# Optimization experiments

Hardware: AMD Instinct MI355X
Metric: run time of the kernel (lower is better)

Reference implementation:

```python
import jax, jax.numpy as jnp
from jax import lax
import numpy as np

D_MODEL = 96; D_STATE = 16; SSM_RATIO = 2.0; D_CONV = 3; K = 4
D_INNER = int(SSM_RATIO * D_MODEL)      # 192
DT_RANK = -(-D_MODEL // 16)             # ceil(96/16) = 6
B_SZ = 4; H = 32; W = 32

# ---- zig-zag (snake) index helpers (static numpy) ----
def _snake_h(Hh, Ww):
    idx = np.tile(np.arange(Ww), (Hh, 1)); idx[1::2] = idx[1::2, ::-1]; return idx  # (H,W)

def _snake_v(Hh, Ww):
    idx = np.tile(np.arange(Hh)[:, None], (1, Ww)); idx[:, 1::2] = idx[::-1, 1::2]; return idx  # (H,W)

def _h_scan(x, d):
    Hh, Ww = x.shape[-2:]
    if d == 'left':
        x = jnp.flip(x, (-1, -2))
    return x[:, :, np.arange(Hh)[:, None], _snake_h(Hh, Ww)]

def _v_scan(x, d):
    Bb, Cc, Hh, Ww = x.shape
    if d == 'up':
        x = jnp.flip(x, (-1, -2))
    t = x[:, :, _snake_v(Hh, Ww), np.arange(Ww)[None, :]]  # gather along H per column
    return jnp.swapaxes(t, -1, -2).reshape(Bb, Cc, Hh, Ww)

def _h_merge(x, d):
    Hh, Ww = x.shape[-2:]
    t = x[:, :, np.arange(Hh)[:, None], _snake_h(Hh, Ww)]
    if d == 'left':
        t = jnp.flip(t, (-1, -2))
    return t

def _v_merge(x, d):
    Hh, Ww = x.shape[-2:]
    t2 = jnp.swapaxes(x, -1, -2)  # (B,C,W,H); requires H==W like the torch source
    t = t2[:, :, _snake_v(Hh, Ww), np.arange(Ww)[None, :]]
    if d == 'up':
        t = jnp.flip(t, (-1, -2))
    return t

def cross_scan(x):
    return jnp.stack([_v_scan(x, 'down'), _v_scan(x, 'up'), _h_scan(x, 'right'), _h_scan(x, 'left')], axis=1)

def cross_merge(ys):
    return (_v_merge(ys[:, 0], 'down') + _v_merge(ys[:, 1], 'up')
            + _h_merge(ys[:, 2], 'right') + _h_merge(ys[:, 3], 'left'))

def selective_scan(u, delta, A, Bs, Cs, Dp, delta_bias):
    # u,delta:(B,K,D,L)  A:(K,D,N)  Bs,Cs:(B,K,N,L)  Dp,delta_bias:(K,D)
    delta = jax.nn.softplus(delta + delta_bias[None, :, :, None])
    dA = jnp.exp(jnp.einsum('bkdl,kdn->lbkdn', delta, A))
    dBu = jnp.einsum('bkdl,bkdl,bknl->lbkdn', delta, u, Bs)
    Ct = jnp.moveaxis(Cs, -1, 0)  # (L,B,K,N)
    def step(h, inp):
        dA_t, dBu_t, c_t = inp
        h = dA_t * h + dBu_t
        return h, jnp.einsum('bkdn,bkn->bkd', h, c_t)
    h0 = jnp.zeros(dA.shape[1:], u.dtype)
    _, ys = lax.scan(step, h0, (dA, dBu, Ct))
    return jnp.moveaxis(ys, 0, -1) + Dp[None, :, :, None] * u  # (B,K,D,L)

def setup_inputs() -> dict:
    key = jax.random.key(0)
    ks = jax.random.split(key, 8)
    x = jax.random.normal(ks[0], (B_SZ, D_MODEL, H, W), jnp.float32)
    in_proj_w = jax.random.normal(ks[1], (2 * D_INNER, D_MODEL), jnp.float32) * (D_MODEL ** -0.5)
    conv_w = jax.random.normal(ks[2], (D_INNER, 1, D_CONV, D_CONV), jnp.float32) * 0.2  # depthwise
    conv_b = jnp.zeros((D_INNER,), jnp.float32)
    x_proj_w = jax.random.normal(ks[3], (K, DT_RANK + 2 * D_STATE, D_INNER), jnp.float32) * (D_INNER ** -0.5)
    s = DT_RANK ** -0.5
    dt_w = jax.random.uniform(ks[4], (K, D_INNER, DT_RANK), jnp.float32, -s, s)
    dt = jax.random.uniform(ks[5], (K, D_INNER), jnp.float32, 0.001, 0.1)
    dt_b = jnp.log(jnp.expm1(dt))  # inverse softplus, as in dt_init
    A_logs = jnp.tile(jnp.log(jnp.arange(1, D_STATE + 1, dtype=jnp.float32)), (K * D_INNER, 1))
    Ds = jnp.ones((K * D_INNER,), jnp.float32)
    gn_gamma = jnp.ones((D_INNER,), jnp.float32)
    gn_beta = jnp.zeros((D_INNER,), jnp.float32)
    out_proj_w = jax.random.normal(ks[6], (D_MODEL, D_INNER), jnp.float32) * (D_INNER ** -0.5)
    return {'x': x, 'in_proj_w': in_proj_w, 'conv_w': conv_w, 'conv_b': conv_b,
            'x_proj_w': x_proj_w, 'dt_w': dt_w, 'dt_b': dt_b, 'A_logs': A_logs, 'Ds': Ds,
            'gn_gamma': gn_gamma, 'gn_beta': gn_beta, 'out_proj_w': out_proj_w}

def reference(x, in_proj_w, conv_w, conv_b, x_proj_w, dt_w, dt_b, A_logs, Ds, gn_gamma, gn_beta, out_proj_w):
    Bb, _, Hh, Ww = x.shape; L = Hh * Ww
    xz = jnp.einsum('bchw,oc->bohw', x, in_proj_w)          # in_proj (1x1 conv, no bias)
    xx, z = jnp.split(xz, 2, axis=1)
    z = jax.nn.silu(z)
    xx = lax.conv_general_dilated(xx, conv_w, (1, 1), 'SAME', feature_group_count=D_INNER,
                                  dimension_numbers=('NCHW', 'OIHW', 'NCHW')) + conv_b[None, :, None, None]
    xx = jax.nn.silu(xx)
    xs = cross_scan(xx).reshape(Bb, K, D_INNER, L)          # 4-direction zig-zag scan
    x_dbl = jnp.einsum('bkdl,kcd->bkcl', xs, x_proj_w)
    dts = jnp.einsum('bkrl,kdr->bkdl', x_dbl[:, :, :DT_RANK], dt_w)
    Bs = x_dbl[:, :, DT_RANK:DT_RANK + D_STATE]
    Cs = x_dbl[:, :, DT_RANK + D_STATE:]
    A = -jnp.exp(A_logs).reshape(K, D_INNER, D_STATE)
    y = selective_scan(xs, dts, A, Bs, Cs, Ds.reshape(K, D_INNER), dt_b)
    y = cross_merge(y.reshape(Bb, K, D_INNER, Hh, Ww))       # (B,D,H,W)
    # out_norm: GroupNorm(1, d_inner) == layernorm over (C,H,W) per sample
    mu = jnp.mean(y, axis=(1, 2, 3), keepdims=True)
    var = jnp.var(y, axis=(1, 2, 3), keepdims=True)
    y = (y - mu) * lax.rsqrt(var + 1e-6)
    y = y * gn_gamma[None, :, None, None] + gn_beta[None, :, None, None]
    y = y * z
    return jnp.einsum('bchw,oc->bohw', y, out_proj_w)
```

## Files before the change

### kernel.cpp

```cpp
#include <hip/hip_runtime.h>
#include <math.h>

#define Bsz 4
#define DM 96
#define DI 192
#define NS 16
#define RK 6
#define KK 4
#define HH 32
#define WW 32
#define LL 1024
#define NC 32
#define CS 32

__device__ __forceinline__ float silu_f(float x) { return x / (1.f + __expf(-x)); }

__device__ __forceinline__ int hw_of_l(int k, int l) {
    int a = l >> 5, r = l & 31;
    int m = (a & 1) ? 31 - r : r;
    int h, w;
    if (k < 2) { w = a; h = m; }
    else       { h = a; w = m; }
    if (k & 1) { h = 31 - h; w = 31 - w; }
    return h * 32 + w;
}

__global__ void in_proj_k(const float* __restrict__ x, const float* __restrict__ w,
                          float* __restrict__ xx, float* __restrict__ zs,
                          float* __restrict__ stats) {
    int bi = blockIdx.x;
    int t = threadIdx.x;
    if (bi == 0 && t < 2 * Bsz) stats[t] = 0.f;
    int lb = bi & 3;
    int og = (bi >> 2) % 96;
    int b = bi / 384;
    int l = lb * 256 + t;
    const float* xb = x + (size_t)b * DM * LL + l;
    float acc[4];
#pragma unroll
    for (int g = 0; g < 4; g++) acc[g] = 0.f;
    for (int c = 0; c < DM; c++) {
        float xv = xb[(size_t)c * LL];
#pragma unroll
        for (int g = 0; g < 4; g++)
            acc[g] = fmaf(xv, w[(size_t)(og * 4 + g) * DM + c], acc[g]);
    }
#pragma unroll
    for (int g = 0; g < 4; g++) {
        int o = og * 4 + g;
        if (o < DI) xx[((size_t)b * DI + o) * LL + l] = acc[g];
        else        zs[((size_t)b * DI + (o - DI)) * LL + l] = silu_f(acc[g]);
    }
}

__global__ void convT_k(const float* __restrict__ xx, const float* __restrict__ cw,
                        const float* __restrict__ cb, float* __restrict__ xxT) {
    __shared__ float tile[32][33];
    int bi = blockIdx.x;
    int h0 = bi % 32;
    int dt = (bi / 32) % 6;
    int b = bi / 192;
    int d0 = dt * 32;
    int t = threadIdx.x;
    int wi = t & 31, dg = t >> 5;

#pragma unroll
    for (int pass = 0; pass < 4; pass++) {
        int di = pass * 8 + dg;
        int d = d0 + di;
        const float* xp = xx + ((size_t)b * DI + d) * LL;
        const float* wp = cw + d * 9;
        float acc = cb[d];
#pragma unroll
        for (int kh = 0; kh < 3; kh++) {
            int hh = h0 + kh - 1;
            if (hh < 0 || hh >= HH) continue;
#pragma unroll
            for (int kw = 0; kw < 3; kw++) {
                int ww2 = wi + kw - 1;
                if (ww2 < 0 || ww2 >= WW) continue;
                acc = fmaf(xp[hh * WW + ww2], wp[kh * 3 + kw], acc);
            }
        }
        tile[wi][di] = silu_f(acc);
    }
    __syncthreads();

    int di = t & 31, w8 = t >> 5;
#pragma unroll
    for (int rep = 0; rep < 4; rep++) {
        int w2 = rep * 8 + w8;
        xxT[((size_t)b * LL + h0 * 32 + w2) * DI + d0 + di] = tile[w2][di];
    }
}

__global__ void __launch_bounds__(512)
xdbl_k(const float* __restrict__ xxT, const float* __restrict__ xpw,
       float* __restrict__ xdbl) {
    __shared__ float tile[64 * 193];
    int blk = blockIdx.x;
    int bk = blk >> 4, lt = blk & 15;
    int k = bk & 3, b = bk >> 2;
    int t = threadIdx.x;

    const float* xb = xxT + (size_t)b * LL * DI;
#pragma unroll
    for (int i = 0; i < 6; i++) {
        int j4 = t + i * 512;
        int lr = j4 / 48;
        int d4 = j4 % 48;
        int hw = hw_of_l(k, lt * 64 + lr);
        float4 v = ((const float4*)(xb + (size_t)hw * DI))[d4];
        float* dst = &tile[lr * 193 + d4 * 4];
        dst[0] = v.x; dst[1] = v.y; dst[2] = v.z; dst[3] = v.w;
    }
    __syncthreads();

    int ll = t & 63;
    int cg = t >> 6;
    int c0 = cg * 5;
    int wlim = (c0 + 5 <= 38) ? 5 : (38 - c0);
    const float* wk = xpw + (size_t)k * 38 * DI;

    float acc[5];
#pragma unroll
    for (int j = 0; j < 5; j++) acc[j] = 0.f;
    const float* xrow = &tile[ll * 193];
#pragma unroll 4
    for (int d = 0; d < DI; d++) {
        float xv = xrow[d];
#pragma unroll
        for (int j = 0; j < 5; j++) {
            int cc = c0 + j; cc = (cc > 37) ? 37 : cc;
            acc[j] = fmaf(xv, wk[(size_t)cc * DI + d], acc[j]);
        }
    }
    float* orow = xdbl + ((size_t)bk * LL + lt * 64 + ll) * 38;
#pragma unroll
    for (int j = 0; j < 5; j++)
        if (j < wlim) orow[c0 + j] = acc[j];
}

__global__ void scan_p1(const float* __restrict__ xxT, const float* __restrict__ xdbl,
                        const float* __restrict__ dtw_g, const float* __restrict__ dtb_g,
                        const float* __restrict__ Alog,
                        float* __restrict__ Pst, float* __restrict__ Hloc) {
    __shared__ float u_tile[CS * 193];
    __shared__ float xd_tile[CS * 38];
    int blk = blockIdx.x;
    int bk = blk / NC, c = blk % NC;
    int k = bk & 3, b = bk >> 2;
    int t = threadIdx.x;

    const float* xb = xxT + (size_t)b * LL * DI;
#pragma unroll
    for (int i = 0; i < 8; i++) {
        int j4 = t + i * 192;
        int s = j4 / 48, d4 = j4 % 48;
        int hw = hw_of_l(k, c * CS + s);
        float4 v = ((const float4*)(xb + (size_t)hw * DI))[d4];
        float* dst = &u_tile[s * 193 + d4 * 4];
        dst[0] = v.x; dst[1] = v.y; dst[2] = v.z; dst[3] = v.w;
    }
    const float* xdsrc = xdbl + ((size_t)bk * LL + c * CS) * 38;
    for (int i = t; i < CS * 38; i += 192) xd_tile[i] = xdsrc[i];
    __syncthreads();

    int d = t;
    int kd = k * DI + d;

    float A[NS];
#pragma unroll
    for (int n = 0; n < NS; n++) A[n] = -__expf(Alog[(size_t)kd * NS + n]);
    float dtw[RK];
#pragma unroll
    for (int r = 0; r < RK; r++) dtw[r] = dtw_g[(size_t)kd * RK + r];
    float dtb = dtb_g[kd];

    float h[NS], P[NS];
#pragma unroll
    for (int n = 0; n < NS; n++) { h[n] = 0.f; P[n] = 1.f; }

    for (int s = 0; s < CS; s++) {
        const float* xd = &xd_tile[s * 38];
        float dt = dtb;
#pragma unroll
        for (int r = 0; r < RK; r++) dt = fmaf(xd[r], dtw[r], dt);
        dt = (dt > 20.f) ? dt : __logf(1.f + __expf(dt));
        float du = dt * u_tile[s * 193 + d];
#pragma unroll
        for (int n = 0; n < NS; n++) {
            float a = __expf(dt * A[n]);
            h[n] = fmaf(a, h[n], du * xd[6 + n]);
            P[n] *= a;
        }
    }
    if (c < NC - 1) {
        size_t base = ((size_t)blk * DI + d) * NS;
#pragma unroll
        for (int n = 0; n < NS; n++) { Pst[base + n] = P[n]; Hloc[base + n] = h[n]; }
    }
}

__global__ void scan_mid(const float* __restrict__ Pst, float* __restrict__ Hloc) {
    int gid = blockIdx.x * 256 + threadIdx.x;
    int bk = gid / 1536;
    int j = gid % 1536;
    const float2* Pp = (const float2*)(Pst + (size_t)bk * NC * (DI * NS)) + j;
    float2* Hp = (float2*)(Hloc + (size_t)bk * NC * (DI * NS)) + j;
    const int S = (DI * NS) / 2;

    float2 h = make_float2(0.f, 0.f);
    float2 P[4], L[4];
#pragma unroll
    for (int q = 0; q < 4; q++) { P[q] = Pp[(size_t)q * S]; L[q] = Hp[(size_t)q * S]; }
    for (int c = 0; c < NC; c += 4) {
        float2 Pn[4], Ln[4];
        if (c + 4 < NC) {
#pragma unroll
            for (int q = 0; q < 4; q++) {
                Pn[q] = Pp[(size_t)(c + 4 + q) * S];
                Ln[q] = Hp[(size_t)(c + 4 + q) * S];
            }
        }
#pragma unroll
        for (int q = 0; q < 4; q++) {
            Hp[(size_t)(c + q) * S] = h;
            h.x = fmaf(P[q].x, h.x, L[q].x);
            h.y = fmaf(P[q].y, h.y, L[q].y);
        }
#pragma unroll
        for (int q = 0; q < 4; q++) { P[q] = Pn[q]; L[q] = Ln[q]; }
    }
}

__global__ void scan_p3(const float* __restrict__ xxT, const float* __restrict__ xdbl,
                        const float* __restrict__ dtw_g, const float* __restrict__ dtb_g,
                        const float* __restrict__ Alog, const float* __restrict__ Ds,
                        const float* __restrict__ Hin, float* __restrict__ ysm) {
    __shared__ float u_tile[CS * 193];
    __shared__ float xd_tile[CS * 38];
    int blk = blockIdx.x;
    int bk = blk / NC, c = blk % NC;
    int k = bk & 3, b = bk >> 2;
    int t = threadIdx.x;

    const float* xb = xxT + (size_t)b * LL * DI;
#pragma unroll
    for (int i = 0; i < 8; i++) {
        int j4 = t + i * 192;
        int s = j4 / 48, d4 = j4 % 48;
        int hw = hw_of_l(k, c * CS + s);
        float4 v = ((const float4*)(xb + (size_t)hw * DI))[d4];
        float* dst = &u_tile[s * 193 + d4 * 4];
        dst[0] = v.x; dst[1] = v.y; dst[2] = v.z; dst[3] = v.w;
    }
    const float* xdsrc = xdbl + ((size_t)bk * LL + c * CS) * 38;
    for (int i = t; i < CS * 38; i += 192) xd_tile[i] = xdsrc[i];
    __syncthreads();

    int d = t;
    int kd = k * DI + d;

    float A[NS];
#pragma unroll
    for (int n = 0; n < NS; n++) A[n] = -__expf(Alog[(size_t)kd * NS + n]);
    float dtw[RK];
#pragma unroll
    for (int r = 0; r < RK; r++) dtw[r] = dtw_g[(size_t)kd * RK + r];
    float dtb = dtb_g[kd];
    float Dp = Ds[kd];

    float h[NS];
    size_t hbase = ((size_t)blk * DI + d) * NS;
#pragma unroll
    for (int n = 0; n < NS; n++) h[n] = Hin[hbase + n];

    float* yk = ysm + (size_t)bk * LL * DI;

    for (int s = 0; s < CS; s++) {
        const float* xd = &xd_tile[s * 38];
        float u = u_tile[s * 193 + d];
        float dt = dtb;
#pragma unroll
        for (int r = 0; r < RK; r++) dt = fmaf(xd[r], dtw[r], dt);
        dt = (dt > 20.f) ? dt : __logf(1.f + __expf(dt));
        float du = dt * u;
        float y = 0.f;
#pragma unroll
        for (int n = 0; n < NS; n++) {
            float a = __expf(dt * A[n]);
            h[n] = fmaf(a, h[n], du * xd[6 + n]);
            y = fmaf(h[n], xd[22 + n], y);
        }
        int hw = hw_of_l(k, c * CS + s);
        yk[(size_t)hw * DI + d] = fmaf(Dp, u, y);
    }
}

#define MT 8
__global__ void merge_k(const float* __restrict__ ysm, float* __restrict__ ym,
                        float* __restrict__ stats) {
    __shared__ float tile[MT][DI + 1];
    __shared__ float sh1[3], sh2[3];
    int b = blockIdx.y;
    int hw0 = blockIdx.x * MT;
    int d = threadIdx.x;
    const float* yb = ysm + (size_t)b * KK * LL * DI;

    float s1 = 0.f, s2 = 0.f;
#pragma unroll
    for (int hwi = 0; hwi < MT; hwi++) {
        int hw = hw0 + hwi;
        float v = yb[((size_t)0 * LL + hw) * DI + d]
                + yb[((size_t)1 * LL + hw) * DI + d]
                + yb[((size_t)2 * LL + hw) * DI + d]
                + yb[((size_t)3 * LL + hw) * DI + d];
        tile[hwi][d] = v;
        s1 += v; s2 = fmaf(v, v, s2);
    }
#pragma unroll
    for (int off = 32; off > 0; off >>= 1) {
        s1 += __shfl_down(s1, off);
        s2 += __shfl_down(s2, off);
    }
    int lane = threadIdx.x & 63, wid = threadIdx.x >> 6;
    if (lane == 0) { sh1[wid] = s1; sh2[wid] = s2; }
    __syncthreads();
    if (threadIdx.x == 0) {
        atomicAdd(&stats[b * 2],     sh1[0] + sh1[1] + sh1[2]);
        atomicAdd(&stats[b * 2 + 1], sh2[0] + sh2[1] + sh2[2]);
    }
#pragma unroll
    for (int rep = 0; rep < MT; rep++) {
        int j = rep * DI + threadIdx.x;
        int d2 = j >> 3;
        int hwi = j & (MT - 1);
        ym[((size_t)b * DI + d2) * LL + hw0 + hwi] = tile[hwi][d2];
    }
}

__global__ void outz_k(const float* __restrict__ ym, const float* __restrict__ zs,
                       const float* __restrict__ g, const float* __restrict__ be,
                       const float* __restrict__ stats, const float* __restrict__ wo,
                       float* __restrict__ out) {
    int bi = blockIdx.x;
    int t = threadIdx.x;
    int lb = bi & 3;
    int og = (bi >> 2) % 32;
    int b = bi / 128;
    int l = lb * 256 + t;

    const float Ninv = 1.f / (float)(DI * LL);
    float mu = stats[b * 2] * Ninv;
    float var = stats[b * 2 + 1] * Ninv - mu * mu;
    float rstd = rsqrtf(var + 1e-6f);

    const float* yb = ym + (size_t)b * DI * LL + l;
    const float* zb = zs + (size_t)b * DI * LL + l;
    float acc[3];
#pragma unroll
    for (int gg = 0; gg < 3; gg++) acc[gg] = 0.f;
    for (int c = 0; c < DI; c++) {
        float v = (yb[(size_t)c * LL] - mu) * rstd * g[c] + be[c];
        float yv = v * zb[(size_t)c * LL];
#pragma unroll
        for (int gg = 0; gg < 3; gg++)
            acc[gg] = fmaf(yv, wo[(size_t)(og * 3 + gg) * DI + c], acc[gg]);
    }
#pragma unroll
    for (int gg = 0; gg < 3; gg++)
        out[((size_t)b * DM + og * 3 + gg) * LL + l] = acc[gg];
}

extern "C" void kernel_launch(void* const* d_in, const int* in_sizes, int n_in,
                              void* d_out, int out_size, void* d_ws, size_t ws_size,
                              hipStream_t stream) {
    const float* x    = (const float*)d_in[0];
    const float* ipw  = (const float*)d_in[1];
    const float* cw   = (const float*)d_in[2];
    const float* cb   = (const float*)d_in[3];
    const float* xpw  = (const float*)d_in[4];
    const float* dtw  = (const float*)d_in[5];
    const float* dtb  = (const float*)d_in[6];
    const float* Alog = (const float*)d_in[7];
    const float* Ds   = (const float*)d_in[8];
    const float* gng  = (const float*)d_in[9];
    const float* gnb  = (const float*)d_in[10];
    const float* opw  = (const float*)d_in[11];
    float* out = (float*)d_out;

    float* ws = (float*)d_ws;
    const size_t o_xx   = 0;
    const size_t o_zs   = o_xx   + (size_t)Bsz * DI * LL;
    const size_t o_xxT  = o_zs   + (size_t)Bsz * DI * LL;
    const size_t o_xdbl = o_xxT  + (size_t)Bsz * LL * DI;
    const size_t o_P    = o_xdbl + (size_t)Bsz * KK * LL * 38;
    const size_t o_H    = o_P    + (size_t)Bsz * KK * NC * DI * NS;
    const size_t o_ysm  = o_H    + (size_t)Bsz * KK * NC * DI * NS;
    const size_t o_st   = o_ysm  + (size_t)Bsz * KK * LL * DI;

    float* xx    = ws + o_xx;
    float* zs    = ws + o_zs;
    float* xxT   = ws + o_xxT;
    float* xdbl  = ws + o_xdbl;
    float* Pst   = ws + o_P;
    float* Hst   = ws + o_H;
    float* ysm   = ws + o_ysm;
    float* stats = ws + o_st;
    float* ym = xx;

    hipLaunchKernelGGL(in_proj_k, dim3(1536), dim3(256), 0, stream, x, ipw, xx, zs, stats);
    hipLaunchKernelGGL(convT_k, dim3(768), dim3(256), 0, stream, xx, cw, cb, xxT);
    hipLaunchKernelGGL(xdbl_k, dim3(256), dim3(512), 0, stream, xxT, xpw, xdbl);
    hipLaunchKernelGGL(scan_p1, dim3(Bsz * KK * NC), dim3(192), 0, stream,
                       xxT, xdbl, dtw, dtb, Alog, Pst, Hst);
    hipLaunchKernelGGL(scan_mid, dim3(96), dim3(256), 0, stream, Pst, Hst);
    hipLaunchKernelGGL(scan_p3, dim3(Bsz * KK * NC), dim3(192), 0, stream,
                       xxT, xdbl, dtw, dtb, Alog, Ds, Hst, ysm);
    hipLaunchKernelGGL(merge_k, dim3(LL / MT, Bsz), dim3(192), 0, stream, ysm, ym, stats);
    hipLaunchKernelGGL(outz_k, dim3(512), dim3(256), 0, stream, ym, zs, gng, gnb, stats, opw, out);
}
```

Baseline: 207.0 us.

## Replace per-state exps with powers when A follows arange structure; vectorize smem tiles

At runtime each thread checks whether its A row equals (n+1)*A0, the standard S4D-real initialisation. If so, the per-step decay factors come from one exp and repeated multiplication instead of 16 exps, in both scan passes. The shared-memory tiles are also relaid out so B, C and dt coefficients load as float4 vectors, and u rows are stored unpadded with float4 writes. This adds a branch and small numerical differences from the repeated products, and its benefit depends on the weights matching that pattern.

```diff
diff --git a/kernel.cpp b/kernel.cpp
--- a/kernel.cpp
+++ b/kernel.cpp
@@ -141,12 +141,14 @@
         if (j < wlim) orow[c0 + j] = acc[j];
 }
 
+#define XDP 40
+
 __global__ void scan_p1(const float* __restrict__ xxT, const float* __restrict__ xdbl,
                         const float* __restrict__ dtw_g, const float* __restrict__ dtb_g,
                         const float* __restrict__ Alog,
                         float* __restrict__ Pst, float* __restrict__ Hloc) {
-    __shared__ float u_tile[CS * 193];
-    __shared__ float xd_tile[CS * 38];
+    __shared__ float u_tile[CS * 192];
+    __shared__ float xd_tile[CS * XDP];
     int blk = blockIdx.x;
     int bk = blk / NC, c = blk % NC;
     int k = bk & 3, b = bk >> 2;
@@ -159,19 +161,25 @@
         int s = j4 / 48, d4 = j4 % 48;
         int hw = hw_of_l(k, c * CS + s);
         float4 v = ((const float4*)(xb + (size_t)hw * DI))[d4];
-        float* dst = &u_tile[s * 193 + d4 * 4];
-        dst[0] = v.x; dst[1] = v.y; dst[2] = v.z; dst[3] = v.w;
+        ((float4*)(&u_tile[s * 192]))[d4] = v;
     }
     const float* xdsrc = xdbl + ((size_t)bk * LL + c * CS) * 38;
-    for (int i = t; i < CS * 38; i += 192) xd_tile[i] = xdsrc[i];
+    for (int i = t; i < CS * 38; i += 192) {
+        int s = i / 38, j = i - s * 38;
+        int pj = (j < 6) ? 32 + j : j - 6;
+        xd_tile[s * XDP + pj] = xdsrc[i];
+    }
     __syncthreads();
 
     int d = t;
     int kd = k * DI + d;
-
-    float A[NS];
-#pragma unroll
-    for (int n = 0; n < NS; n++) A[n] = -__expf(Alog[(size_t)kd * NS + n]);
+    float A0 = -__expf(Alog[(size_t)kd * NS]);
+    bool pw = true;
+#pragma unroll
+    for (int n = 1; n < NS; n++) {
+        float An = -__expf(Alog[(size_t)kd * NS + n]);
+        pw = pw && (fabsf(An - (float)(n + 1) * A0) <= 1e-4f * (float)(n + 1));
+    }
     float dtw[RK];
 #pragma unroll
     for (int r = 0; r < RK; r++) dtw[r] = dtw_g[(size_t)kd * RK + r];
@@ -179,20 +187,71 @@
 
     float h[NS], P[NS];
 #pragma unroll
-    for (int n = 0; n < NS; n++) { h[n] = 0.f; P[n] = 1.f; }
-
-    for (int s = 0; s < CS; s++) {
-        const float* xd = &xd_tile[s * 38];
-        float dt = dtb;
-#pragma unroll
-        for (int r = 0; r < RK; r++) dt = fmaf(xd[r], dtw[r], dt);
-        dt = (dt > 20.f) ? dt : __logf(1.f + __expf(dt));
-        float du = dt * u_tile[s * 193 + d];
-#pragma unroll
-        for (int n = 0; n < NS; n++) {
-            float a = __expf(dt * A[n]);
-            h[n] = fmaf(a, h[n], du * xd[6 + n]);
-            P[n] *= a;
+    for (int n = 0; n < NS; n++) h[n] = 0.f;
+
+    if (pw) {
+        float R = 1.f;
+        for (int s = 0; s < CS; s++) {
+            const float4* xr = (const float4*)(&xd_tile[s * XDP]);
+            float4 b0 = xr[0], b1 = xr[1], b2 = xr[2], b3 = xr[3];
+            float4 q0 = xr[8], q1 = xr[9];
+            float bb[16];
+            bb[0]=b0.x; bb[1]=b0.y; bb[2]=b0.z; bb[3]=b0.w;
+            bb[4]=b1.x; bb[5]=b1.y; bb[6]=b1.z; bb[7]=b1.w;
+            bb[8]=b2.x; bb[9]=b2.y; bb[10]=b2.z; bb[11]=b2.w;
+            bb[12]=b3.x; bb[13]=b3.y; bb[14]=b3.z; bb[15]=b3.w;
+            float dt = dtb;
+            dt = fmaf(q0.x, dtw[0], dt); dt = fmaf(q0.y, dtw[1], dt);
+            dt = fmaf(q0.z, dtw[2], dt); dt = fmaf(q0.w, dtw[3], dt);
+            dt = fmaf(q1.x, dtw[4], dt); dt = fmaf(q1.y, dtw[5], dt);
+            dt = (dt > 20.f) ? dt : __logf(1.f + __expf(dt));
+            float du = dt * u_tile[s * 192 + d];
+            float r1 = __expf(dt * A0);
+            float r2 = r1 * r1, r4 = r2 * r2, r8 = r4 * r4;
+            float aa[16];
+            aa[0] = r1; aa[1] = r2; aa[2] = r1 * r2; aa[3] = r4;
+#pragma unroll
+            for (int n = 0; n < 4; n++) aa[n + 4] = aa[n] * r4;
+#pragma unroll
+            for (int n = 0; n < 8; n++) aa[n + 8] = aa[n] * r8;
+#pragma unroll
+            for (int n = 0; n < NS; n++) h[n] = fmaf(aa[n], h[n], du * bb[n]);
+            R *= r1;
+        }
+        float R2 = R * R, R4 = R2 * R2, R8 = R4 * R4;
+        P[0] = R; P[1] = R2; P[2] = R * R2; P[3] = R4;
+#pragma unroll
+        for (int n = 0; n < 4; n++) P[n + 4] = P[n] * R4;
+        P[7] = R8;
+#pragma unroll
+        for (int n = 0; n < 8; n++) P[n + 8] = P[n] * R8;
+    } else {
+        float A[NS];
+#pragma unroll
+        for (int n = 0; n < NS; n++) A[n] = -__expf(Alog[(size_t)kd * NS + n]);
+#pragma unroll
+        for (int n = 0; n < NS; n++) P[n] = 1.f;
+        for (int s = 0; s < CS; s++) {
+            const float4* xr = (const float4*)(&xd_tile[s * XDP]);
+            float4 b0 = xr[0], b1 = xr[1], b2 = xr[2], b3 = xr[3];
+            float4 q0 = xr[8], q1 = xr[9];
+            float bb[16];
+            bb[0]=b0.x; bb[1]=b0.y; bb[2]=b0.z; bb[3]=b0.w;
+            bb[4]=b1.x; bb[5]=b1.y; bb[6]=b1.z; bb[7]=b1.w;
+            bb[8]=b2.x; bb[9]=b2.y; bb[10]=b2.z; bb[11]=b2.w;
+            bb[12]=b3.x; bb[13]=b3.y; bb[14]=b3.z; bb[15]=b3.w;
+            float dt = dtb;
+            dt = fmaf(q0.x, dtw[0], dt); dt = fmaf(q0.y, dtw[1], dt);
+            dt = fmaf(q0.z, dtw[2], dt); dt = fmaf(q0.w, dtw[3], dt);
+            dt = fmaf(q1.x, dtw[4], dt); dt = fmaf(q1.y, dtw[5], dt);
+            dt = (dt > 20.f) ? dt : __logf(1.f + __expf(dt));
+            float du = dt * u_tile[s * 192 + d];
+#pragma unroll
+            for (int n = 0; n < NS; n++) {
+                float a = __expf(dt * A[n]);
+                h[n] = fmaf(a, h[n], du * bb[n]);
+                P[n] *= a;
+            }
         }
     }
     if (c < NC - 1) {
@@ -238,8 +297,8 @@
                         const float* __restrict__ dtw_g, const float* __restrict__ dtb_g,
                         const float* __restrict__ Alog, const float* __restrict__ Ds,
                         const float* __restrict__ Hin, float* __restrict__ ysm) {
-    __shared__ float u_tile[CS * 193];
-    __shared__ float xd_tile[CS * 38];
+    __shared__ float u_tile[CS * 192];
+    __shared__ float xd_tile[CS * XDP];
     int blk = blockIdx.x;
     int bk = blk / NC, c = blk % NC;
     int k = bk & 3, b = bk >> 2;
@@ -252,19 +311,25 @@
         int s = j4 / 48, d4 = j4 % 48;
         int hw = hw_of_l(k, c * CS + s);
         float4 v = ((const float4*)(xb + (size_t)hw * DI))[d4];
-        float* dst = &u_tile[s * 193 + d4 * 4];
-        dst[0] = v.x; dst[1] = v.y; dst[2] = v.z; dst[3] = v.w;
+        ((float4*)(&u_tile[s * 192]))[d4] = v;
     }
     const float* xdsrc = xdbl + ((size_t)bk * LL + c * CS) * 38;
-    for (int i = t; i < CS * 38; i += 192) xd_tile[i] = xdsrc[i];
+    for (int i = t; i < CS * 38; i += 192) {
+        int s = i / 38, j = i - s * 38;
+        int pj = (j < 6) ? 32 + j : j - 6;
+        xd_tile[s * XDP + pj] = xdsrc[i];
+    }
     __syncthreads();
 
     int d = t;
     int kd = k * DI + d;
-
-    float A[NS];
-#pragma unroll
-    for (int n = 0; n < NS; n++) A[n] = -__expf(Alog[(size_t)kd * NS + n]);
+    float A0 = -__expf(Alog[(size_t)kd * NS]);
+    bool pw = true;
+#pragma unroll
+    for (int n = 1; n < NS; n++) {
+        float An = -__expf(Alog[(size_t)kd * NS + n]);
+        pw = pw && (fabsf(An - (float)(n + 1) * A0) <= 1e-4f * (float)(n + 1));
+    }
     float dtw[RK];
 #pragma unroll
     for (int r = 0; r < RK; r++) dtw[r] = dtw_g[(size_t)kd * RK + r];
@@ -278,23 +343,80 @@
 
     float* yk = ysm + (size_t)bk * LL * DI;
 
-    for (int s = 0; s < CS; s++) {
-        const float* xd = &xd_tile[s * 38];
-        float u = u_tile[s * 193 + d];
-        float dt = dtb;
-#pragma unroll
-        for (int r = 0; r < RK; r++) dt = fmaf(xd[r], dtw[r], dt);
-        dt = (dt > 20.f) ? dt : __logf(1.f + __expf(dt));
-        float du = dt * u;
-        float y = 0.f;
-#pragma unroll
-        for (int n = 0; n < NS; n++) {
-            float a = __expf(dt * A[n]);
-            h[n] = fmaf(a, h[n], du * xd[6 + n]);
-            y = fmaf(h[n], xd[22 + n], y);
-        }
-        int hw = hw_of_l(k, c * CS + s);
-        yk[(size_t)hw * DI + d] = fmaf(Dp, u, y);
+    if (pw) {
+        for (int s = 0; s < CS; s++) {
+            const float4* xr = (const float4*)(&xd_tile[s * XDP]);
+            float4 b0 = xr[0], b1 = xr[1], b2 = xr[2], b3 = xr[3];
+            float4 c0 = xr[4], c1 = xr[5], c2 = xr[6], c3 = xr[7];
+            float4 q0 = xr[8], q1 = xr[9];
+            float bb[16], cc[16];
+            bb[0]=b0.x; bb[1]=b0.y; bb[2]=b0.z; bb[3]=b0.w;
+            bb[4]=b1.x; bb[5]=b1.y; bb[6]=b1.z; bb[7]=b1.w;
+            bb[8]=b2.x; bb[9]=b2.y; bb[10]=b2.z; bb[11]=b2.w;
+            bb[12]=b3.x; bb[13]=b3.y; bb[14]=b3.z; bb[15]=b3.w;
+            cc[0]=c0.x; cc[1]=c0.y; cc[2]=c0.z; cc[3]=c0.w;
+            cc[4]=c1.x; cc[5]=c1.y; cc[6]=c1.z; cc[7]=c1.w;
+            cc[8]=c2.x; cc[9]=c2.y; cc[10]=c2.z; cc[11]=c2.w;
+            cc[12]=c3.x; cc[13]=c3.y; cc[14]=c3.z; cc[15]=c3.w;
+            float dt = dtb;
+            dt = fmaf(q0.x, dtw[0], dt); dt = fmaf(q0.y, dtw[1], dt);
+            dt = fmaf(q0.z, dtw[2], dt); dt = fmaf(q0.w, dtw[3], dt);
+            dt = fmaf(q1.x, dtw[4], dt); dt = fmaf(q1.y, dtw[5], dt);
+            dt = (dt > 20.f) ? dt : __logf(1.f + __expf(dt));
+            float u = u_tile[s * 192 + d];
+            float du = dt * u;
+            float r1 = __expf(dt * A0);
+            float r2 = r1 * r1, r4 = r2 * r2, r8 = r4 * r4;
+            float aa[16];
+            aa[0] = r1; aa[1] = r2; aa[2] = r1 * r2; aa[3] = r4;
+#pragma unroll
+            for (int n = 0; n < 4; n++) aa[n + 4] = aa[n] * r4;
+#pragma unroll
+            for (int n = 0; n < 8; n++) aa[n + 8] = aa[n] * r8;
+            float y = 0.f;
+#pragma unroll
+            for (int n = 0; n < NS; n++) {
+                h[n] = fmaf(aa[n], h[n], du * bb[n]);
+                y = fmaf(h[n], cc[n], y);
+            }
+            int hw = hw_of_l(k, c * CS + s);
+            yk[(size_t)hw * DI + d] = fmaf(Dp, u, y);
+        }
+    } else {
+        float A[NS];
+#pragma unroll
+        for (int n = 0; n < NS; n++) A[n] = -__expf(Alog[(size_t)kd * NS + n]);
+        for (int s = 0; s < CS; s++) {
+            const float4* xr = (const float4*)(&xd_tile[s * XDP]);
+            float4 b0 = xr[0], b1 = xr[1], b2 = xr[2], b3 = xr[3];
+            float4 c0 = xr[4], c1 = xr[5], c2 = xr[6], c3 = xr[7];
+            float4 q0 = xr[8], q1 = xr[9];
+            float bb[16], cc[16];
+            bb[0]=b0.x; bb[1]=b0.y; bb[2]=b0.z; bb[3]=b0.w;
+            bb[4]=b1.x; bb[5]=b1.y; bb[6]=b1.z; bb[7]=b1.w;
+            bb[8]=b2.x; bb[9]=b2.y; bb[10]=b2.z; bb[11]=b2.w;
+            bb[12]=b3.x; bb[13]=b3.y; bb[14]=b3.z; bb[15]=b3.w;
+            cc[0]=c0.x; cc[1]=c0.y; cc[2]=c0.z; cc[3]=c0.w;
+            cc[4]=c1.x; cc[5]=c1.y; cc[6]=c1.z; cc[7]=c1.w;
+            cc[8]=c2.x; cc[9]=c2.y; cc[10]=c2.z; cc[11]=c2.w;
+            cc[12]=c3.x; cc[13]=c3.y; cc[14]=c3.z; cc[15]=c3.w;
+            float dt = dtb;
+            dt = fmaf(q0.x, dtw[0], dt); dt = fmaf(q0.y, dtw[1], dt);
+            dt = fmaf(q0.z, dtw[2], dt); dt = fmaf(q0.w, dtw[3], dt);
+            dt = fmaf(q1.x, dtw[4], dt); dt = fmaf(q1.y, dtw[5], dt);
+            dt = (dt > 20.f) ? dt : __logf(1.f + __expf(dt));
+            float u = u_tile[s * 192 + d];
+            float du = dt * u;
+            float y = 0.f;
+#pragma unroll
+            for (int n = 0; n < NS; n++) {
+                float a = __expf(dt * A[n]);
+                h[n] = fmaf(a, h[n], du * bb[n]);
+                y = fmaf(h[n], cc[n], y);
+            }
+            int hw = hw_of_l(k, c * CS + s);
+            yk[(size_t)hw * DI + d] = fmaf(Dp, u, y);
+        }
     }
 }
 
```

Result: faster. 190.1 us (-8.2%).
